# Kernel optimization log

Measured on AMD Instinct MI355X. Metric: run time of the kernel, lower is better.

The kernel has to match this reference:

```python
import jax, jax.numpy as jnp
import numpy as np

N_NODES = 50000
N_EDGES = 800000
F_NODE = 128
F_EDGE = 32
H = 64


def _gat_layer(x, row, col, e_emb, W, le_W, att_src, att_dst, att_edge, bias):
    """PyG GATConv (heads=1, concat=True) with edge_dim, incl. self loops.
    x: [N, Fin]; row/col: [E] int (src, dst); e_emb: [E, H].
    """
    N = x.shape[0]
    loop = jnp.arange(N, dtype=row.dtype)
    row_a = jnp.concatenate([row, loop])
    col_a = jnp.concatenate([col, loop])
    # self-loop edge attr = mean of edge embeddings (PyG fill_value='mean')
    e_mean = jnp.mean(e_emb, axis=0)
    e_all = jnp.concatenate([e_emb, jnp.broadcast_to(e_mean, (N, e_emb.shape[1]))], axis=0)

    h = x @ W.T                      # [N, H]
    a_src = h @ att_src              # [N]
    a_dst = h @ att_dst              # [N]
    a_edge = (e_all @ le_W.T) @ att_edge  # [E+N]

    alpha = jax.nn.leaky_relu(a_src[row_a] + a_dst[col_a] + a_edge, negative_slope=0.2)
    # segment softmax over destination node neighborhoods
    m = jax.ops.segment_max(alpha, col_a, num_segments=N)
    ex = jnp.exp(alpha - m[col_a])
    denom = jax.ops.segment_sum(ex, col_a, num_segments=N)
    w = ex / denom[col_a]            # [E+N]
    out = jax.ops.segment_sum(h[row_a] * w[:, None], col_a, num_segments=N)
    return out + bias


def setup_inputs() -> dict:
    key = jax.random.key(0)
    ks = jax.random.split(key, 20)
    s = 0.1
    inp = {
        "x": jax.random.normal(ks[0], (N_NODES, F_NODE), dtype=jnp.float32),
        "edge_attr": jax.random.normal(ks[1], (N_EDGES, F_EDGE), dtype=jnp.float32),
        "edge_index": jax.random.randint(ks[2], (2, N_EDGES), 0, N_NODES, dtype=jnp.int32),
        # edge encoder (Linear with bias)
        "enc_W": jax.random.normal(ks[3], (H, F_EDGE), dtype=jnp.float32) * s,
        "enc_b": jnp.zeros((H,), dtype=jnp.float32),
        # conv1 params
        "W1": jax.random.normal(ks[4], (H, F_NODE), dtype=jnp.float32) * s,
        "le1_W": jax.random.normal(ks[5], (H, H), dtype=jnp.float32) * s,
        "as1": jax.random.normal(ks[6], (H,), dtype=jnp.float32) * s,
        "ad1": jax.random.normal(ks[7], (H,), dtype=jnp.float32) * s,
        "ae1": jax.random.normal(ks[8], (H,), dtype=jnp.float32) * s,
        "b1": jnp.zeros((H,), dtype=jnp.float32),
        # conv2 params
        "W2": jax.random.normal(ks[9], (H, H), dtype=jnp.float32) * s,
        "le2_W": jax.random.normal(ks[10], (H, H), dtype=jnp.float32) * s,
        "as2": jax.random.normal(ks[11], (H,), dtype=jnp.float32) * s,
        "ad2": jax.random.normal(ks[12], (H,), dtype=jnp.float32) * s,
        "ae2": jax.random.normal(ks[13], (H,), dtype=jnp.float32) * s,
        "b2": jnp.zeros((H,), dtype=jnp.float32),
        # edge scorer MLP: Linear(2H, H) -> ReLU -> Linear(H, 1)
        "s1_W": jax.random.normal(ks[14], (H, 2 * H), dtype=jnp.float32) * s,
        "s1_b": jnp.zeros((H,), dtype=jnp.float32),
        "s2_W": jax.random.normal(ks[15], (1, H), dtype=jnp.float32) * s,
        "s2_b": jnp.zeros((1,), dtype=jnp.float32),
    }
    return inp


def reference(x, edge_attr, edge_index, enc_W, enc_b,
              W1, le1_W, as1, ad1, ae1, b1,
              W2, le2_W, as2, ad2, ae2, b2,
              s1_W, s1_b, s2_W, s2_b):
    row, col = edge_index[0], edge_index[1]
    edge_emb = edge_attr @ enc_W.T + enc_b           # [E, H]
    h = jax.nn.relu(_gat_layer(x, row, col, edge_emb, W1, le1_W, as1, ad1, ae1, b1))
    # dropout p=0.5 is identity in eval mode
    h = _gat_layer(h, row, col, edge_emb, W2, le2_W, as2, ad2, ae2, b2)
    ef = jnp.concatenate([h[row], h[col]], axis=1)   # [E, 2H]
    z = jax.nn.relu(ef @ s1_W.T + s1_b) @ s2_W.T + s2_b  # [E, 1]
    return jax.nn.sigmoid(z).squeeze(-1)             # [E]
```

## Files before the change

kernel.cpp:

```cpp
#include <hip/hip_runtime.h>
#include <cstdint>
#include <cstddef>

#define NN 50000
#define NE 800000
#define FN 128
#define FE 32
#define HD 64
#define SCAN_NB ((NN + 255) / 256)
#define EP_NB (NE / 256)
#define GM_NB ((NN + 63) / 64)

typedef float vfloat4 __attribute__((ext_vector_type(4)));

__device__ __forceinline__ float lrelu(float x) { return x > 0.f ? x : 0.2f * x; }

__device__ __forceinline__ unsigned omap(float f) {
  unsigned u = __float_as_uint(f);
  return (u & 0x80000000u) ? ~u : (u | 0x80000000u);
}
__device__ __forceinline__ float odec(unsigned u) {
  return __uint_as_float((u & 0x80000000u) ? (u ^ 0x80000000u) : ~u);
}

__global__ __launch_bounds__(256) void k_small0(const float* __restrict__ le1W, const float* __restrict__ ae1,
                         const float* __restrict__ le2W, const float* __restrict__ ae2,
                         const float* __restrict__ encW, const float* __restrict__ encb,
                         const float* __restrict__ s1W,
                         float* __restrict__ small, float* __restrict__ Scomb,
                         int* __restrict__ counts) {
  int t = threadIdx.x;
  if (blockIdx.x > 0) {
    int i = (blockIdx.x - 1) * 256 + t;
    if (i < NN) counts[i] = 0;
    return;
  }
  __shared__ float sv1[64], sv2[64];
  if (t < 64) {
    float v1 = 0.f, v2 = 0.f;
    for (int j = 0; j < 64; ++j) {
      v1 += le1W[j * 64 + t] * ae1[j];
      v2 += le2W[j * 64 + t] * ae2[j];
    }
    sv1[t] = v1; sv2[t] = v2;
    small[t] = v1; small[64 + t] = v2;
    float cb1 = encb[t] * v1, cb2 = encb[t] * v2;
    #pragma unroll
    for (int m = 32; m; m >>= 1) { cb1 += __shfl_xor(cb1, m); cb2 += __shfl_xor(cb2, m); }
    if (t == 0) { small[192] = cb1; small[193] = cb2; }
  }
  __syncthreads();
  if (t < 32) {
    float p1 = 0.f, p2 = 0.f;
    for (int i = 0; i < 64; ++i) {
      p1 += encW[i * 32 + t] * sv1[i];
      p2 += encW[i * 32 + t] * sv2[i];
    }
    small[128 + t] = p1; small[160 + t] = p2;
  }
  if (t < 64) {
    for (int j = 0; j < 64; ++j) {
      Scomb[j * 64 + t] = s1W[j * 128 + t];
      Scomb[(64 + j) * 64 + t] = s1W[j * 128 + 64 + t];
    }
  }
}

__global__ __launch_bounds__(256) void k_scanA(const int* __restrict__ counts,
                                               int* __restrict__ loc, int* __restrict__ blocksums) {
  int tid = threadIdx.x;
  int i = blockIdx.x * 256 + tid;
  int v = (i < NN) ? counts[i] : 0;
  int lane = tid & 63, wid = tid >> 6;
  int x = v;
  #pragma unroll
  for (int d = 1; d < 64; d <<= 1) {
    int y = __shfl_up(x, d);
    if (lane >= d) x += y;
  }
  __shared__ int ws[4], wpref[4];
  if (lane == 63) ws[wid] = x;
  __syncthreads();
  if (tid == 0) {
    int run = 0;
    #pragma unroll
    for (int w = 0; w < 4; ++w) { wpref[w] = run; run += ws[w]; }
    blocksums[blockIdx.x] = run;
  }
  __syncthreads();
  if (i < NN) loc[i] = x - v + wpref[wid];
}

__global__ __launch_bounds__(256) void k_scanBC(const int* __restrict__ blocksums,
                                                int* __restrict__ offa,
                                                float* __restrict__ small) {
  __shared__ int sb[SCAN_NB];
  int tid = threadIdx.x;
  if (tid < SCAN_NB) sb[tid] = blocksums[tid];
  __syncthreads();
  int pre = 0;
  for (int b = 0; b < blockIdx.x; ++b) pre += sb[b];
  int i = blockIdx.x * 256 + tid;
  if (i < NN) offa[i] += pre;
  if (blockIdx.x == 0 && tid == 0) {
    int tot = 0;
    for (int b = 0; b < SCAN_NB; ++b) tot += sb[b];
    offa[NN] = tot;
    small[194] = small[228] * (1.0f / NE);
    small[195] = small[229] * (1.0f / NE);
  }
}

__global__ __launch_bounds__(256) void k_fused0(const float* __restrict__ attr,
                                                const int* __restrict__ col,
                                                const float* __restrict__ small,
                                                float* __restrict__ a_e1, float* __restrict__ a_e2,
                                                int* __restrict__ rank,
                                                int* __restrict__ counts,
                                                float* __restrict__ sums,
                                                unsigned* __restrict__ maxi,
                                                const float* __restrict__ x, const float* __restrict__ W1,
                                                float* __restrict__ h1,
                                                const float* __restrict__ as, const float* __restrict__ ad,
                                                float* __restrict__ asrc, float* __restrict__ adst) {
  __shared__ float smem[8704];
  int tid = threadIdx.x;
  if (blockIdx.x < EP_NB) {
    float* sattr = smem;
    float* redbuf = smem + 8448;
    float sp1[32], sp2[32];
    #pragma unroll
    for (int j = 0; j < 8; ++j) {
      float4 v1 = ((const float4*)(small + 128))[j];
      float4 v2 = ((const float4*)(small + 160))[j];
      sp1[j*4+0] = v1.x; sp1[j*4+1] = v1.y; sp1[j*4+2] = v1.z; sp1[j*4+3] = v1.w;
      sp2[j*4+0] = v2.x; sp2[j*4+1] = v2.y; sp2[j*4+2] = v2.z; sp2[j*4+3] = v2.w;
    }
    float c1 = small[192], c2 = small[193];
    int e = blockIdx.x * 256 + tid;
    int c = col[e];
    const vfloat4* ain = (const vfloat4*)(attr + (size_t)blockIdx.x * 256 * FE);
    #pragma unroll
    for (int it = 0; it < 8; ++it) {
      int idx = it * 256 + tid;
      vfloat4 v = __builtin_nontemporal_load(ain + idx);
      int r = idx >> 3, ch = idx & 7;
      float* dst = &sattr[r * 33 + ch * 4];
      dst[0] = v.x; dst[1] = v.y; dst[2] = v.z; dst[3] = v.w;
    }
    __syncthreads();
    const float* myrow = &sattr[tid * 33];
    float d1 = c1, d2 = c2;
    #pragma unroll
    for (int j = 0; j < 32; ++j) {
      float a = myrow[j];
      d1 += a * sp1[j];
      d2 += a * sp2[j];
    }
    a_e1[e] = d1;
    a_e2[e] = d2;
    rank[e] = atomicAdd(&counts[c], 1);
    float s1 = d1, s2 = d2, m1 = d1, m2 = d2;
    #pragma unroll
    for (int m = 32; m; m >>= 1) {
      s1 += __shfl_xor(s1, m); s2 += __shfl_xor(s2, m);
      m1 = fmaxf(m1, __shfl_xor(m1, m)); m2 = fmaxf(m2, __shfl_xor(m2, m));
    }
    int wid = tid >> 6;
    if ((tid & 63) == 0) { redbuf[wid] = s1; redbuf[4 + wid] = s2; redbuf[8 + wid] = m1; redbuf[12 + wid] = m2; }
    __syncthreads();
    if (tid == 0) atomicAdd(&sums[0], redbuf[0] + redbuf[1] + redbuf[2] + redbuf[3]);
    if (tid == 1) atomicAdd(&sums[1], redbuf[4] + redbuf[5] + redbuf[6] + redbuf[7]);
    if (tid == 2) atomicMax(&maxi[2], omap(fmaxf(fmaxf(redbuf[8], redbuf[9]), fmaxf(redbuf[10], redbuf[11]))));
    if (tid == 3) atomicMax(&maxi[3], omap(fmaxf(fmaxf(redbuf[12], redbuf[13]), fmaxf(redbuf[14], redbuf[15]))));
  } else {
    float (*At)[68] = (float(*)[68])smem;
    float (*Bt)[68] = (float(*)[68])(smem + 4352);
    int m0 = (blockIdx.x - EP_NB) * 64;
    float acc[4][4] = {};
    for (int kc = 0; kc < 128; kc += 64) {
      #pragma unroll
      for (int it = 0; it < 4; ++it) {
        int idx = it * 256 + tid;
        int m = idx & 63, kv = idx >> 6;
        float4 bv = ((const float4*)(W1 + (size_t)m * 128 + kc))[kv];
        Bt[kv*4+0][m] = bv.x; Bt[kv*4+1][m] = bv.y; Bt[kv*4+2][m] = bv.z; Bt[kv*4+3][m] = bv.w;
        int gm = m0 + m;
        float4 av = make_float4(0.f, 0.f, 0.f, 0.f);
        if (gm < NN) av = ((const float4*)(x + (size_t)gm * 128 + kc))[kv];
        At[kv*4+0][m] = av.x; At[kv*4+1][m] = av.y; At[kv*4+2][m] = av.z; At[kv*4+3][m] = av.w;
      }
      __syncthreads();
      int tn = tid & 15, tm = tid >> 4;
      #pragma unroll 8
      for (int k = 0; k < 64; ++k) {
        float4 a4 = *(const float4*)&At[k][tm * 4];
        float4 b4 = *(const float4*)&Bt[k][tn * 4];
        acc[0][0] += a4.x*b4.x; acc[0][1] += a4.x*b4.y; acc[0][2] += a4.x*b4.z; acc[0][3] += a4.x*b4.w;
        acc[1][0] += a4.y*b4.x; acc[1][1] += a4.y*b4.y; acc[1][2] += a4.y*b4.z; acc[1][3] += a4.y*b4.w;
        acc[2][0] += a4.z*b4.x; acc[2][1] += a4.z*b4.y; acc[2][2] += a4.z*b4.z; acc[2][3] += a4.z*b4.w;
        acc[3][0] += a4.w*b4.x; acc[3][1] += a4.w*b4.y; acc[3][2] += a4.w*b4.z; acc[3][3] += a4.w*b4.w;
      }
      __syncthreads();
    }
    int tn = tid & 15, tm = tid >> 4;
    #pragma unroll
    for (int i = 0; i < 4; ++i) {
      int gm = m0 + tm * 4 + i;
      if (gm < NN) {
        float4 o = make_float4(acc[i][0], acc[i][1], acc[i][2], acc[i][3]);
        *(float4*)(h1 + (size_t)gm * 64 + tn * 4) = o;
      }
    }
    __shared__ float wmax[4];
    float4 asv = ((const float4*)as)[tn];
    float4 adv = ((const float4*)ad)[tn];
    float smax = -1e30f;
    #pragma unroll
    for (int i = 0; i < 4; ++i) {
      float s = acc[i][0]*asv.x + acc[i][1]*asv.y + acc[i][2]*asv.z + acc[i][3]*asv.w;
      float d = acc[i][0]*adv.x + acc[i][1]*adv.y + acc[i][2]*adv.z + acc[i][3]*adv.w;
      #pragma unroll
      for (int m = 8; m; m >>= 1) { s += __shfl_xor(s, m, 16); d += __shfl_xor(d, m, 16); }
      int gm = m0 + tm * 4 + i;
      if (tn == 0 && gm < NN) { asrc[gm] = s; adst[gm] = d; smax = fmaxf(smax, s); }
    }
    #pragma unroll
    for (int m = 32; m; m >>= 1) smax = fmaxf(smax, __shfl_xor(smax, m));
    if ((tid & 63) == 0) wmax[tid >> 6] = smax;
    __syncthreads();
    if (tid == 0)
      atomicMax(&maxi[0], omap(fmaxf(fmaxf(wmax[0], wmax[1]), fmaxf(wmax[2], wmax[3]))));
  }
}

__global__ __launch_bounds__(256) void k_scatter(const int* __restrict__ row, const int* __restrict__ col,
                                                 const float* __restrict__ a_e1, const float* __restrict__ a_e2,
                                                 const int* __restrict__ rank, const int* __restrict__ offa,
                                                 int4* __restrict__ pk) {
  int t = blockIdx.x * 256 + threadIdx.x;
  if (t >= NE / 4) return;
  int e0 = t, e1 = t + NE / 4, e2 = t + NE / 2, e3 = t + 3 * (NE / 4);
  int c0 = col[e0], c1 = col[e1], c2 = col[e2], c3 = col[e3];
  int r0 = rank[e0], r1 = rank[e1], r2 = rank[e2], r3 = rank[e3];
  int o0 = offa[c0], o1 = offa[c1], o2 = offa[c2], o3 = offa[c3];
  int4 q0, q1, q2, q3;
  q0.x = row[e0]; q0.y = __float_as_int(a_e1[e0]); q0.z = __float_as_int(a_e2[e0]); q0.w = e0;
  q1.x = row[e1]; q1.y = __float_as_int(a_e1[e1]); q1.z = __float_as_int(a_e2[e1]); q1.w = e1;
  q2.x = row[e2]; q2.y = __float_as_int(a_e1[e2]); q2.z = __float_as_int(a_e2[e2]); q2.w = e2;
  q3.x = row[e3]; q3.y = __float_as_int(a_e1[e3]); q3.z = __float_as_int(a_e2[e3]); q3.w = e3;
  pk[o0 + r0] = q0;
  pk[o1 + r1] = q1;
  pk[o2 + r2] = q2;
  pk[o3 + r3] = q3;
}

template <int K, int ASD>
__global__ __launch_bounds__(256) void k_gemm(const float* __restrict__ A, const float* __restrict__ B,
                                              float* __restrict__ C, int M, int ldc,
                                              const float* __restrict__ as, const float* __restrict__ ad,
                                              float* __restrict__ asrc, float* __restrict__ adst,
                                              unsigned* __restrict__ maxslot) {
  __shared__ float At[64][68];
  __shared__ float Bt[64][68];
  int tid = threadIdx.x;
  int m0 = blockIdx.x * 64;
  const float* Bp = B + (size_t)blockIdx.y * 64 * K;
  float acc[4][4] = {};
  for (int kc = 0; kc < K; kc += 64) {
    #pragma unroll
    for (int it = 0; it < 4; ++it) {
      int idx = it * 256 + tid;
      int m = idx & 63, kv = idx >> 6;
      float4 bv = ((const float4*)(Bp + (size_t)m * K + kc))[kv];
      Bt[kv*4+0][m] = bv.x; Bt[kv*4+1][m] = bv.y; Bt[kv*4+2][m] = bv.z; Bt[kv*4+3][m] = bv.w;
      int gm = m0 + m;
      float4 av = make_float4(0.f, 0.f, 0.f, 0.f);
      if (gm < M) av = ((const float4*)(A + (size_t)gm * K + kc))[kv];
      At[kv*4+0][m] = av.x; At[kv*4+1][m] = av.y; At[kv*4+2][m] = av.z; At[kv*4+3][m] = av.w;
    }
    __syncthreads();
    int tn = tid & 15, tm = tid >> 4;
    #pragma unroll 8
    for (int k = 0; k < 64; ++k) {
      float4 a4 = *(const float4*)&At[k][tm * 4];
      float4 b4 = *(const float4*)&Bt[k][tn * 4];
      acc[0][0] += a4.x*b4.x; acc[0][1] += a4.x*b4.y; acc[0][2] += a4.x*b4.z; acc[0][3] += a4.x*b4.w;
      acc[1][0] += a4.y*b4.x; acc[1][1] += a4.y*b4.y; acc[1][2] += a4.y*b4.z; acc[1][3] += a4.y*b4.w;
      acc[2][0] += a4.z*b4.x; acc[2][1] += a4.z*b4.y; acc[2][2] += a4.z*b4.z; acc[2][3] += a4.z*b4.w;
      acc[3][0] += a4.w*b4.x; acc[3][1] += a4.w*b4.y; acc[3][2] += a4.w*b4.z; acc[3][3] += a4.w*b4.w;
    }
    __syncthreads();
  }
  int tn = tid & 15, tm = tid >> 4;
  #pragma unroll
  for (int i = 0; i < 4; ++i) {
    int gm = m0 + tm * 4 + i;
    if (gm < M) {
      float4 o = make_float4(acc[i][0], acc[i][1], acc[i][2], acc[i][3]);
      *(float4*)(C + (size_t)gm * ldc + blockIdx.y * 64 + tn * 4) = o;
    }
  }
  if constexpr (ASD) {
    __shared__ float wmax[4];
    float4 asv = ((const float4*)as)[tn];
    float4 adv = ((const float4*)ad)[tn];
    float smax = -1e30f;
    #pragma unroll
    for (int i = 0; i < 4; ++i) {
      float s = acc[i][0]*asv.x + acc[i][1]*asv.y + acc[i][2]*asv.z + acc[i][3]*asv.w;
      float d = acc[i][0]*adv.x + acc[i][1]*adv.y + acc[i][2]*adv.z + acc[i][3]*adv.w;
      #pragma unroll
      for (int m = 8; m; m >>= 1) { s += __shfl_xor(s, m, 16); d += __shfl_xor(d, m, 16); }
      int gm = m0 + tm * 4 + i;
      if (tn == 0 && gm < M) { asrc[gm] = s; adst[gm] = d; smax = fmaxf(smax, s); }
    }
    #pragma unroll
    for (int m = 32; m; m >>= 1) smax = fmaxf(smax, __shfl_xor(smax, m));
    if ((tid & 63) == 0) wmax[tid >> 6] = smax;
    __syncthreads();
    if (tid == 0)
      atomicMax(maxslot, omap(fmaxf(fmaxf(wmax[0], wmax[1]), fmaxf(wmax[2], wmax[3]))));
  }
}

__global__ __launch_bounds__(256) void k_agg(const float* __restrict__ h, const int* __restrict__ offa,
                                             const int4* __restrict__ pk, int comp,
                                             const float* __restrict__ asrc, const float* __restrict__ adst,
                                             const float* __restrict__ small, int selfIdx,
                                             const unsigned* __restrict__ maxi,
                                             const float* __restrict__ bias, float* __restrict__ outp,
                                             int do_relu) {
  int gt = blockIdx.x * 256 + threadIdx.x;
  int n = gt >> 6, lane = gt & 63;
  if (n >= NN) return;
  int beg = offa[n], end = offa[n + 1];
  float adn = adst[n];
  float mx = lrelu(odec(maxi[comp]) + adn + odec(maxi[2 + comp]));
  float alpha_self = lrelu(asrc[n] + adn + small[selfIdx]);
  float ex_self = __expf(alpha_self - mx);
  float denom = ex_self;
  float acc0 = ex_self * h[(size_t)n * 64 + lane];
  float acc1 = 0.f, acc2 = 0.f, acc3 = 0.f;
  float acc4 = 0.f, acc5 = 0.f, acc6 = 0.f, acc7 = 0.f;
  for (int base = beg; base < end; base += 64) {
    int p = base + lane;
    int cnt = min(64, end - base);
    float ex = 0.f; int s = 0;
    if (p < end) {
      int4 q = pk[p];
      s = q.x;
      float ae = __int_as_float(comp ? q.z : q.y);
      ex = __expf(lrelu(asrc[s] + adn + ae) - mx);
    }
    float exs = ex;
    #pragma unroll
    for (int m = 32; m; m >>= 1) exs += __shfl_xor(exs, m);
    denom += exs;
    int q8 = cnt & ~7;
    int q = 0;
    for (; q < q8; q += 8) {
      float e0 = __shfl(ex, q),     e1 = __shfl(ex, q + 1);
      float e2 = __shfl(ex, q + 2), e3 = __shfl(ex, q + 3);
      float e4 = __shfl(ex, q + 4), e5 = __shfl(ex, q + 5);
      float e6 = __shfl(ex, q + 6), e7 = __shfl(ex, q + 7);
      int s0 = __shfl(s, q),     s1 = __shfl(s, q + 1);
      int s2 = __shfl(s, q + 2), s3 = __shfl(s, q + 3);
      int s4 = __shfl(s, q + 4), s5 = __shfl(s, q + 5);
      int s6 = __shfl(s, q + 6), s7 = __shfl(s, q + 7);
      acc0 += e0 * h[(size_t)s0 * 64 + lane];
      acc1 += e1 * h[(size_t)s1 * 64 + lane];
      acc2 += e2 * h[(size_t)s2 * 64 + lane];
      acc3 += e3 * h[(size_t)s3 * 64 + lane];
      acc4 += e4 * h[(size_t)s4 * 64 + lane];
      acc5 += e5 * h[(size_t)s5 * 64 + lane];
      acc6 += e6 * h[(size_t)s6 * 64 + lane];
      acc7 += e7 * h[(size_t)s7 * 64 + lane];
    }
    int q4 = cnt & ~3;
    if (q < q4) {
      float e0 = __shfl(ex, q),     e1 = __shfl(ex, q + 1);
      float e2 = __shfl(ex, q + 2), e3 = __shfl(ex, q + 3);
      int s0 = __shfl(s, q),     s1 = __shfl(s, q + 1);
      int s2 = __shfl(s, q + 2), s3 = __shfl(s, q + 3);
      acc0 += e0 * h[(size_t)s0 * 64 + lane];
      acc1 += e1 * h[(size_t)s1 * 64 + lane];
      acc2 += e2 * h[(size_t)s2 * 64 + lane];
      acc3 += e3 * h[(size_t)s3 * 64 + lane];
      q = q4;
    }
    for (; q < cnt; ++q) {
      float eq = __shfl(ex, q);
      int sq = __shfl(s, q);
      acc0 += eq * h[(size_t)sq * 64 + lane];
    }
  }
  float r = ((acc0 + acc1) + (acc2 + acc3)) + ((acc4 + acc5) + (acc6 + acc7));
  r = r / denom + bias[lane];
  if (do_relu) r = fmaxf(r, 0.f);
  outp[(size_t)n * 64 + lane] = r;
}

__global__ __launch_bounds__(256) void k_final(const int* __restrict__ offa, const int4* __restrict__ pk,
                                               const float* __restrict__ uv, const float* __restrict__ s1b,
                                               const float* __restrict__ s2w, const float* __restrict__ s2b,
                                               float* __restrict__ outp) {
  int gt = blockIdx.x * 256 + threadIdx.x;
  int n = gt >> 6, lane = gt & 63;
  if (n >= NN) return;
  int g = lane >> 4, i = lane & 15;
  int beg = offa[n], end = offa[n + 1];
  float4 v4 = ((const float4*)(uv + (size_t)n * 128 + 64))[i];
  float4 bb = ((const float4*)s1b)[i];
  float4 ww = ((const float4*)s2w)[i];
  float4 vb = make_float4(v4.x + bb.x, v4.y + bb.y, v4.z + bb.z, v4.w + bb.w);
  float sb = s2b[0];
  int p = beg + g;
  for (; p + 4 < end; p += 8) {
    int4 qa = pk[p];
    int4 qb = pk[p + 4];
    float4 ua = ((const float4*)(uv + (size_t)qa.x * 128))[i];
    float4 ub = ((const float4*)(uv + (size_t)qb.x * 128))[i];
    float za = fmaxf(ua.x + vb.x, 0.f) * ww.x + fmaxf(ua.y + vb.y, 0.f) * ww.y
             + fmaxf(ua.z + vb.z, 0.f) * ww.z + fmaxf(ua.w + vb.w, 0.f) * ww.w;
    float zb = fmaxf(ub.x + vb.x, 0.f) * ww.x + fmaxf(ub.y + vb.y, 0.f) * ww.y
             + fmaxf(ub.z + vb.z, 0.f) * ww.z + fmaxf(ub.w + vb.w, 0.f) * ww.w;
    #pragma unroll
    for (int m = 1; m < 16; m <<= 1) { za += __shfl_xor(za, m, 16); zb += __shfl_xor(zb, m, 16); }
    if (i == 0) {
      outp[qa.w] = 1.f / (1.f + __expf(-(za + sb)));
      outp[qb.w] = 1.f / (1.f + __expf(-(zb + sb)));
    }
  }
  if (p < end) {
    int4 q = pk[p];
    float4 u = ((const float4*)(uv + (size_t)q.x * 128))[i];
    float z = fmaxf(u.x + vb.x, 0.f) * ww.x + fmaxf(u.y + vb.y, 0.f) * ww.y
            + fmaxf(u.z + vb.z, 0.f) * ww.z + fmaxf(u.w + vb.w, 0.f) * ww.w;
    #pragma unroll
    for (int m = 1; m < 16; m <<= 1) z += __shfl_xor(z, m, 16);
    if (i == 0) outp[q.w] = 1.f / (1.f + __expf(-(z + sb)));
  }
}

extern "C" void kernel_launch(void* const* d_in, const int* in_sizes, int n_in,
                              void* d_out, int out_size, void* d_ws, size_t ws_size,
                              hipStream_t stream) {
  const float* x    = (const float*)d_in[0];
  const float* attr = (const float*)d_in[1];
  const int*   eidx = (const int*)d_in[2];
  const float* encW = (const float*)d_in[3];
  const float* encb = (const float*)d_in[4];
  const float* W1   = (const float*)d_in[5];
  const float* le1W = (const float*)d_in[6];
  const float* as1  = (const float*)d_in[7];
  const float* ad1  = (const float*)d_in[8];
  const float* ae1w = (const float*)d_in[9];
  const float* b1   = (const float*)d_in[10];
  const float* W2   = (const float*)d_in[11];
  const float* le2W = (const float*)d_in[12];
  const float* as2  = (const float*)d_in[13];
  const float* ad2  = (const float*)d_in[14];
  const float* ae2w = (const float*)d_in[15];
  const float* b2   = (const float*)d_in[16];
  const float* s1W  = (const float*)d_in[17];
  const float* s1b  = (const float*)d_in[18];
  const float* s2w  = (const float*)d_in[19];
  const float* s2b  = (const float*)d_in[20];
  float* outp = (float*)d_out;

  const int* row = eidx;
  const int* col = eidx + NE;

  char* p = (char*)d_ws;
  auto alloc = [&](size_t bytes) { char* r = p; p += (bytes + 255) & ~(size_t)255; return r; };
  float* small = (float*)alloc(1024);
  unsigned* maxi = (unsigned*)alloc(256);
  float* Scomb = (float*)alloc(8192 * 4);
  int*   counts= (int*)alloc((size_t)NN * 4);
  int*   offa  = (int*)alloc((size_t)(NN + 1) * 4);
  int*   bsums = (int*)alloc((size_t)SCAN_NB * 4);
  float* a_e1  = (float*)alloc((size_t)NE * 4);
  float* a_e2  = (float*)alloc((size_t)NE * 4);
  int*   rank  = (int*)alloc((size_t)NE * 4);
  int4*  pk    = (int4*)alloc((size_t)NE * 16);
  float* h1    = (float*)alloc((size_t)NN * 64 * 4);
  float* out1  = (float*)alloc((size_t)NN * 64 * 4);
  float* h2    = (float*)alloc((size_t)NN * 64 * 4);
  float* out2  = (float*)alloc((size_t)NN * 64 * 4);
  float* asrc1 = (float*)alloc((size_t)NN * 4);
  float* adst1 = (float*)alloc((size_t)NN * 4);
  float* asrc2 = (float*)alloc((size_t)NN * 4);
  float* adst2 = (float*)alloc((size_t)NN * 4);
  float* uv = h1;

  hipMemsetAsync(small, 0, 1280, stream);

  k_small0<<<SCAN_NB + 1, 256, 0, stream>>>(le1W, ae1w, le2W, ae2w, encW, encb, s1W, small, Scomb, counts);
  k_fused0<<<EP_NB + GM_NB, 256, 0, stream>>>(attr, col, small, a_e1, a_e2, rank, counts,
                                              small + 228, maxi, x, W1, h1, as1, ad1, asrc1, adst1);
  k_scanA<<<SCAN_NB, 256, 0, stream>>>(counts, offa, bsums);
  k_scanBC<<<SCAN_NB, 256, 0, stream>>>(bsums, offa, small);
  k_scatter<<<(NE / 4 + 255) / 256, 256, 0, stream>>>(row, col, a_e1, a_e2, rank, offa, pk);

  k_agg<<<(NN * 64) / 256, 256, 0, stream>>>(h1, offa, pk, 0, asrc1, adst1,
                                             small, 194, maxi, b1, out1, 1);
  k_gemm<64, 1><<<dim3((NN + 63) / 64, 1), 256, 0, stream>>>(out1, W2, h2, NN, 64, as2, ad2, asrc2, adst2, maxi + 1);
  k_agg<<<(NN * 64) / 256, 256, 0, stream>>>(h2, offa, pk, 1, asrc2, adst2,
                                             small, 195, maxi, b2, out2, 0);
  k_gemm<64, 0><<<dim3((NN + 63) / 64, 2), 256, 0, stream>>>(out2, Scomb, uv, NN, 128, nullptr, nullptr, nullptr, nullptr, nullptr);
  k_final<<<(NN * 64) / 256, 256, 0, stream>>>(offa, pk, uv, s1b, s2w, s2b, outp);
}
```

Measured before the change: 300.6 us.

## Count degrees first and scatter packed edges directly from fused edge kernel

Degree counting moves into the first small kernel, with counts zeroed by a memset. The scan now runs before the edge-projection kernel and also writes a cursor array. The edge kernel then uses an atomic on the cursor to place each packed record (src, two attention logits, edge id) straight into CSR order. This removes the separate scatter kernel and the intermediate a_e1/a_e2/rank arrays, cutting a launch and roughly 10 MB of extra global traffic. The cost is a second pass reading col, a stricter serial dependency, and non-deterministic order within each segment.

```diff
diff --git a/kernel.cpp b/kernel.cpp
--- a/kernel.cpp
+++ b/kernel.cpp
@@ -28,11 +28,11 @@
                          const float* __restrict__ encW, const float* __restrict__ encb,
                          const float* __restrict__ s1W,
                          float* __restrict__ small, float* __restrict__ Scomb,
-                         int* __restrict__ counts) {
+                         const int* __restrict__ col, int* __restrict__ counts) {
   int t = threadIdx.x;
   if (blockIdx.x > 0) {
-    int i = (blockIdx.x - 1) * 256 + t;
-    if (i < NN) counts[i] = 0;
+    int e = (blockIdx.x - 1) * 256 + t;
+    atomicAdd(&counts[col[e]], 1);
     return;
   }
   __shared__ float sv1[64], sv2[64];
@@ -93,7 +93,7 @@
 
 __global__ __launch_bounds__(256) void k_scanBC(const int* __restrict__ blocksums,
                                                 int* __restrict__ offa,
-                                                float* __restrict__ small) {
+                                                int* __restrict__ cur) {
   __shared__ int sb[SCAN_NB];
   int tid = threadIdx.x;
   if (tid < SCAN_NB) sb[tid] = blocksums[tid];
@@ -101,22 +101,24 @@
   int pre = 0;
   for (int b = 0; b < blockIdx.x; ++b) pre += sb[b];
   int i = blockIdx.x * 256 + tid;
-  if (i < NN) offa[i] += pre;
+  if (i < NN) {
+    int off = offa[i] + pre;
+    offa[i] = off;
+    cur[i] = off;
+  }
   if (blockIdx.x == 0 && tid == 0) {
     int tot = 0;
     for (int b = 0; b < SCAN_NB; ++b) tot += sb[b];
     offa[NN] = tot;
-    small[194] = small[228] * (1.0f / NE);
-    small[195] = small[229] * (1.0f / NE);
   }
 }
 
 __global__ __launch_bounds__(256) void k_fused0(const float* __restrict__ attr,
+                                                const int* __restrict__ row,
                                                 const int* __restrict__ col,
                                                 const float* __restrict__ small,
-                                                float* __restrict__ a_e1, float* __restrict__ a_e2,
-                                                int* __restrict__ rank,
-                                                int* __restrict__ counts,
+                                                int* __restrict__ cur,
+                                                int4* __restrict__ pk,
                                                 float* __restrict__ sums,
                                                 unsigned* __restrict__ maxi,
                                                 const float* __restrict__ x, const float* __restrict__ W1,
@@ -139,13 +141,14 @@
     float c1 = small[192], c2 = small[193];
     int e = blockIdx.x * 256 + tid;
     int c = col[e];
+    int r = row[e];
     const vfloat4* ain = (const vfloat4*)(attr + (size_t)blockIdx.x * 256 * FE);
     #pragma unroll
     for (int it = 0; it < 8; ++it) {
       int idx = it * 256 + tid;
       vfloat4 v = __builtin_nontemporal_load(ain + idx);
-      int r = idx >> 3, ch = idx & 7;
-      float* dst = &sattr[r * 33 + ch * 4];
+      int rr = idx >> 3, ch = idx & 7;
+      float* dst = &sattr[rr * 33 + ch * 4];
       dst[0] = v.x; dst[1] = v.y; dst[2] = v.z; dst[3] = v.w;
     }
     __syncthreads();
@@ -157,9 +160,13 @@
       d1 += a * sp1[j];
       d2 += a * sp2[j];
     }
-    a_e1[e] = d1;
-    a_e2[e] = d2;
-    rank[e] = atomicAdd(&counts[c], 1);
+    int p = atomicAdd(&cur[c], 1);
+    int4 q;
+    q.x = r;
+    q.y = __float_as_int(d1);
+    q.z = __float_as_int(d2);
+    q.w = e;
+    pk[p] = q;
     float s1 = d1, s2 = d2, m1 = d1, m2 = d2;
     #pragma unroll
     for (int m = 32; m; m >>= 1) {
@@ -234,27 +241,6 @@
   }
 }
 
-__global__ __launch_bounds__(256) void k_scatter(const int* __restrict__ row, const int* __restrict__ col,
-                                                 const float* __restrict__ a_e1, const float* __restrict__ a_e2,
-                                                 const int* __restrict__ rank, const int* __restrict__ offa,
-                                                 int4* __restrict__ pk) {
-  int t = blockIdx.x * 256 + threadIdx.x;
-  if (t >= NE / 4) return;
-  int e0 = t, e1 = t + NE / 4, e2 = t + NE / 2, e3 = t + 3 * (NE / 4);
-  int c0 = col[e0], c1 = col[e1], c2 = col[e2], c3 = col[e3];
-  int r0 = rank[e0], r1 = rank[e1], r2 = rank[e2], r3 = rank[e3];
-  int o0 = offa[c0], o1 = offa[c1], o2 = offa[c2], o3 = offa[c3];
-  int4 q0, q1, q2, q3;
-  q0.x = row[e0]; q0.y = __float_as_int(a_e1[e0]); q0.z = __float_as_int(a_e2[e0]); q0.w = e0;
-  q1.x = row[e1]; q1.y = __float_as_int(a_e1[e1]); q1.z = __float_as_int(a_e2[e1]); q1.w = e1;
-  q2.x = row[e2]; q2.y = __float_as_int(a_e1[e2]); q2.z = __float_as_int(a_e2[e2]); q2.w = e2;
-  q3.x = row[e3]; q3.y = __float_as_int(a_e1[e3]); q3.z = __float_as_int(a_e2[e3]); q3.w = e3;
-  pk[o0 + r0] = q0;
-  pk[o1 + r1] = q1;
-  pk[o2 + r2] = q2;
-  pk[o3 + r3] = q3;
-}
-
 template <int K, int ASD>
 __global__ __launch_bounds__(256) void k_gemm(const float* __restrict__ A, const float* __restrict__ B,
                                               float* __restrict__ C, int M, int ldc,
@@ -327,7 +313,7 @@
 __global__ __launch_bounds__(256) void k_agg(const float* __restrict__ h, const int* __restrict__ offa,
                                              const int4* __restrict__ pk, int comp,
                                              const float* __restrict__ asrc, const float* __restrict__ adst,
-                                             const float* __restrict__ small, int selfIdx,
+                                             const float* __restrict__ small,
                                              const unsigned* __restrict__ maxi,
                                              const float* __restrict__ bias, float* __restrict__ outp,
                                              int do_relu) {
@@ -337,7 +323,8 @@
   int beg = offa[n], end = offa[n + 1];
   float adn = adst[n];
   float mx = lrelu(odec(maxi[comp]) + adn + odec(maxi[2 + comp]));
-  float alpha_self = lrelu(asrc[n] + adn + small[selfIdx]);
+  float a_self = small[228 + comp] * (1.0f / NE);
+  float alpha_self = lrelu(asrc[n] + adn + a_self);
   float ex_self = __expf(alpha_self - mx);
   float denom = ex_self;
   float acc0 = ex_self * h[(size_t)n * 64 + lane];
@@ -479,10 +466,8 @@
   float* Scomb = (float*)alloc(8192 * 4);
   int*   counts= (int*)alloc((size_t)NN * 4);
   int*   offa  = (int*)alloc((size_t)(NN + 1) * 4);
+  int*   cur   = (int*)alloc((size_t)NN * 4);
   int*   bsums = (int*)alloc((size_t)SCAN_NB * 4);
-  float* a_e1  = (float*)alloc((size_t)NE * 4);
-  float* a_e2  = (float*)alloc((size_t)NE * 4);
-  int*   rank  = (int*)alloc((size_t)NE * 4);
   int4*  pk    = (int4*)alloc((size_t)NE * 16);
   float* h1    = (float*)alloc((size_t)NN * 64 * 4);
   float* out1  = (float*)alloc((size_t)NN * 64 * 4);
@@ -495,19 +480,19 @@
   float* uv = h1;
 
   hipMemsetAsync(small, 0, 1280, stream);
-
-  k_small0<<<SCAN_NB + 1, 256, 0, stream>>>(le1W, ae1w, le2W, ae2w, encW, encb, s1W, small, Scomb, counts);
-  k_fused0<<<EP_NB + GM_NB, 256, 0, stream>>>(attr, col, small, a_e1, a_e2, rank, counts,
+  hipMemsetAsync(counts, 0, (size_t)NN * 4, stream);
+
+  k_small0<<<EP_NB + 1, 256, 0, stream>>>(le1W, ae1w, le2W, ae2w, encW, encb, s1W, small, Scomb, col, counts);
+  k_scanA<<<SCAN_NB, 256, 0, stream>>>(counts, offa, bsums);
+  k_scanBC<<<SCAN_NB, 256, 0, stream>>>(bsums, offa, cur);
+  k_fused0<<<EP_NB + GM_NB, 256, 0, stream>>>(attr, row, col, small, cur, pk,
                                               small + 228, maxi, x, W1, h1, as1, ad1, asrc1, adst1);
-  k_scanA<<<SCAN_NB, 256, 0, stream>>>(counts, offa, bsums);
-  k_scanBC<<<SCAN_NB, 256, 0, stream>>>(bsums, offa, small);
-  k_scatter<<<(NE / 4 + 255) / 256, 256, 0, stream>>>(row, col, a_e1, a_e2, rank, offa, pk);
 
   k_agg<<<(NN * 64) / 256, 256, 0, stream>>>(h1, offa, pk, 0, asrc1, adst1,
-                                             small, 194, maxi, b1, out1, 1);
+                                             small, maxi, b1, out1, 1);
   k_gemm<64, 1><<<dim3((NN + 63) / 64, 1), 256, 0, stream>>>(out1, W2, h2, NN, 64, as2, ad2, asrc2, adst2, maxi + 1);
   k_agg<<<(NN * 64) / 256, 256, 0, stream>>>(h2, offa, pk, 1, asrc2, adst2,
-                                             small, 195, maxi, b2, out2, 0);
+                                             small, maxi, b2, out2, 0);
   k_gemm<64, 0><<<dim3((NN + 63) / 64, 2), 256, 0, stream>>>(out2, Scomb, uv, NN, 128, nullptr, nullptr, nullptr, nullptr, nullptr);
   k_final<<<(NN * 64) / 256, 256, 0, stream>>>(offa, pk, uv, s1b, s2w, s2b, outp);
 }
```

Measured after the change: 314.4 us. 1.05x slower.
